# Kernel tuning notes

Measured on AMD Instinct MI355X. Metric: run time of the kernel, lower is better.

## Reference

```python
import jax, jax.numpy as jnp
import numpy as np

B, T, D, H, L, FF, SPLIT = 2, 4096, 256, 4 * 0 + 8, 4, 1024, 2048
HD = D // H
EPS = 1e-5


def _layernorm(x, s, b):
    mu = jnp.mean(x, axis=-1, keepdims=True)
    var = jnp.mean(jnp.square(x - mu), axis=-1, keepdims=True)
    return (x - mu) * jax.lax.rsqrt(var + EPS) * s + b


def setup_inputs() -> dict:
    key = jax.random.key(0)
    ks = jax.random.split(key, 10)
    sc = 0.02
    inp = {
        "rows": jax.random.normal(ks[0], (B, T, D), jnp.float32),
        "train_target_embeddings": jax.random.normal(ks[1], (B, SPLIT, D), jnp.float32),
        "Wq": sc * jax.random.normal(ks[2], (L, D, D), jnp.float32),
        "bq": jnp.zeros((L, D), jnp.float32),
        "Wk": sc * jax.random.normal(ks[3], (L, D, D), jnp.float32),
        "bk": jnp.zeros((L, D), jnp.float32),
        "Wv": sc * jax.random.normal(ks[4], (L, D, D), jnp.float32),
        "bv": jnp.zeros((L, D), jnp.float32),
        "Wo": sc * jax.random.normal(ks[5], (L, D, D), jnp.float32),
        "bo": jnp.zeros((L, D), jnp.float32),
        "W1": sc * jax.random.normal(ks[6], (L, D, FF), jnp.float32),
        "b1": jnp.zeros((L, FF), jnp.float32),
        "W2": sc * jax.random.normal(ks[7], (L, FF, D), jnp.float32),
        "b2": jnp.zeros((L, D), jnp.float32),
        "ln1_s": jnp.ones((L, D), jnp.float32),
        "ln1_b": jnp.zeros((L, D), jnp.float32),
        "ln2_s": jnp.ones((L, D), jnp.float32),
        "ln2_b": jnp.zeros((L, D), jnp.float32),
        "split": SPLIT,
    }
    return inp


def reference(rows, train_target_embeddings, Wq, bq, Wk, bk, Wv, bv, Wo, bo,
              W1, b1, W2, b2, ln1_s, ln1_b, ln2_s, ln2_b, split):
    # residual add of train target embeddings onto the train rows
    x = rows.at[:, :split, :].add(train_target_embeddings)
    t = x.shape[1]
    # allowed mask: every query can see all train columns; test queries also see themselves
    key_is_train = jnp.arange(t) < split                      # [T]
    allowed = key_is_train[None, :] | jnp.eye(t, dtype=bool)  # [T,T]
    neg = jnp.asarray(-1e9, x.dtype)
    scale = 1.0 / np.sqrt(HD)
    n_layers = Wq.shape[0]
    for l in range(n_layers):
        # multi-head attention with structured mask
        q = (x @ Wq[l] + bq[l]).reshape(x.shape[0], t, H, HD)
        k = (x @ Wk[l] + bk[l]).reshape(x.shape[0], t, H, HD)
        v = (x @ Wv[l] + bv[l]).reshape(x.shape[0], t, H, HD)
        logits = jnp.einsum('bqhd,bkhd->bhqk', q, k) * scale
        logits = jnp.where(allowed[None, None], logits, neg)
        attn = jax.nn.softmax(logits, axis=-1)
        o = jnp.einsum('bhqk,bkhd->bqhd', attn, v).reshape(x.shape[0], t, D)
        x = _layernorm(x + (o @ Wo[l] + bo[l]), ln1_s[l], ln1_b[l])
        # feed-forward
        h = jax.nn.gelu(x @ W1[l] + b1[l])
        x = _layernorm(x + (h @ W2[l] + b2[l]), ln2_s[l], ln2_b[l])
    return x
```

## Files before the change

kernel.cpp:

```cpp
#include <hip/hip_runtime.h>
#include <cstdint>
#include <cstddef>

#define TSEQ 4096
#define BATCH 2
#define DIM 256
#define NHEAD 8
#define HDIM 32
#define NLAYER 4
#define FFDIM 1024
#define SPLITN 2048
#define MROWS (BATCH * TSEQ)

#define QSCALE 0.2550784545f

typedef __attribute__((ext_vector_type(4))) float f32x4;
typedef __attribute__((ext_vector_type(8))) short bf16x8;

__device__ __forceinline__ short f2bf(float f) {
  union { float f; uint32_t u; } v; v.f = f;
  uint32_t r = v.u + 0x7fffu + ((v.u >> 16) & 1u);
  return (short)(r >> 16);
}

__device__ __forceinline__ float bf2f(short s) {
  union { uint32_t u; float f; } v; v.u = ((uint32_t)(uint16_t)s) << 16;
  return v.f;
}

__device__ __forceinline__ float fast_exp2(float x) {
#if __has_builtin(__builtin_amdgcn_exp2f)
  return __builtin_amdgcn_exp2f(x);
#else
  float r;
  asm volatile("v_exp_f32 %0, %1\n\ts_nop 1" : "=v"(r) : "v"(x));
  return r;
#endif
}

__device__ __forceinline__ uint32_t pack2bf(float a, float b) {
  union { float f; uint32_t u; } ua, ub; ua.f = a; ub.f = b;
  return ((ua.u + 0x8000u) >> 16) | ((ub.u + 0x8000u) & 0xffff0000u);
}

__device__ __forceinline__ float gelu_f(float x) {
  float u = 0.7978845608f * x * (1.0f + 0.044715f * x * x);
  u = fminf(fmaxf(u, -20.f), 20.f);
  float e = fast_exp2(2.885390082f * u);
  float t = (e - 1.0f) / (e + 1.0f);
  return 0.5f * x * (1.0f + t);
}

#define AS1 __attribute__((address_space(1)))
#define AS3 __attribute__((address_space(3)))
__device__ __forceinline__ void gload16(const void* g, void* l) {
  __builtin_amdgcn_global_load_lds((AS1 void*)g, (AS3 void*)l, 16, 0, 0);
}

__global__ __launch_bounds__(256) void prep_w(
    const float* __restrict__ Wq, const float* __restrict__ Wk,
    const float* __restrict__ Wv, const float* __restrict__ Wo,
    const float* __restrict__ W1, const float* __restrict__ W2,
    short* __restrict__ qkvT, short* __restrict__ woT,
    short* __restrict__ w1T, short* __restrict__ w2T)
{
  const int NQKV = NLAYER * 768 * DIM;
  const int NO   = NLAYER * DIM * DIM;
  const int NF   = NLAYER * FFDIM * DIM;
  const int total = NQKV + NO + 2 * NF;
  for (int idx = blockIdx.x * 256 + threadIdx.x; idx < total; idx += gridDim.x * 256) {
    if (idx < NQKV) {
      const int l = idx / (768 * DIM);
      const int rem = idx - l * 768 * DIM;
      const int n = rem >> 8, k = rem & 255;
      const float* src = (n < 256) ? Wq : ((n < 512) ? Wk : Wv);
      qkvT[idx] = f2bf(src[((size_t)l * DIM + k) * DIM + (n & 255)]);
    } else if (idx < NQKV + NO) {
      const int j = idx - NQKV;
      const int l = j >> 16;
      const int rem = j & 65535;
      const int n = rem >> 8, k = rem & 255;
      woT[j] = f2bf(Wo[((size_t)l * DIM + k) * DIM + n]);
    } else if (idx < NQKV + NO + NF) {
      const int j = idx - NQKV - NO;
      const int l = j >> 18;
      const int rem = j & 262143;
      const int n = rem >> 8, k = rem & 255;
      w1T[j] = f2bf(W1[((size_t)l * DIM + k) * FFDIM + n]);
    } else {
      const int j = idx - NQKV - NO - NF;
      const int l = j >> 18;
      const int rem = j & 262143;
      const int n = rem >> 10, k = rem & 1023;
      w2T[j] = f2bf(W2[((size_t)l * FFDIM + k) * DIM + n]);
    }
  }
}

__global__ __launch_bounds__(256) void prep_x(
    const float* __restrict__ rows, const float* __restrict__ tte,
    float* __restrict__ xf, short* __restrict__ xb)
{
  const size_t idx = (size_t)blockIdx.x * 256 + threadIdx.x;
  float4 v = ((const float4*)rows)[idx];
  const size_t e = idx * 4;
  const int m = (int)(e >> 8);
  const int d = (int)(e & 255);
  const int t = m & (TSEQ - 1);
  const int bb = m >> 12;
  if (t < SPLITN) {
    const float4 a = ((const float4*)tte)[((size_t)bb * SPLITN + t) * (DIM / 4) + (d >> 2)];
    v.x += a.x; v.y += a.y; v.z += a.z; v.w += a.w;
  }
  ((float4*)xf)[idx] = v;
  short4 pk; pk.x = f2bf(v.x); pk.y = f2bf(v.y); pk.z = f2bf(v.z); pk.w = f2bf(v.w);
  ((short4*)xb)[idx] = pk;
}

#define GBM 128
#define GBN 64
#define GBK 64

template<int EPI>
__global__ __launch_bounds__(256, 4) void gemm_bt(
    const short* __restrict__ A, const short* __restrict__ BT,
    const float* __restrict__ bias0, const float* __restrict__ bias1,
    const float* __restrict__ bias2, void* __restrict__ Cout,
    int M, int N, int K)
{
  __shared__ short As[GBM * GBK];
  __shared__ short Bs[GBN * GBK];
  const int tid = threadIdx.x;
  const int lane = tid & 63;
  const int wave = tid >> 6;
  const int wm = wave & 1, wn = wave >> 1;
  const int col = lane & 15, quad = lane >> 4;

  const short* Ab = A + (size_t)blockIdx.x * GBM * K;
  const short* Bb = BT + (size_t)blockIdx.y * GBN * K;

  const f32x4 fz = {0.f, 0.f, 0.f, 0.f};
  f32x4 acc[4][2];
#pragma unroll
  for (int i = 0; i < 4; ++i)
#pragma unroll
    for (int j = 0; j < 2; ++j) acc[i][j] = fz;

  for (int k0 = 0; k0 < K; k0 += GBK) {
#pragma unroll
    for (int p = 0; p < 4; ++p) {
      int i = p * 256 + tid;
      gload16(Ab + (size_t)(i >> 3) * K + k0 + (i & 7) * 8, &As[i * 8]);
    }
#pragma unroll
    for (int p = 0; p < 2; ++p) {
      int i = p * 256 + tid;
      gload16(Bb + (size_t)(i >> 3) * K + k0 + (i & 7) * 8, &Bs[i * 8]);
    }
    __syncthreads();
#pragma unroll
    for (int ks = 0; ks < GBK; ks += 32) {
      bf16x8 af[4], bfr[2];
#pragma unroll
      for (int tm = 0; tm < 4; ++tm)
        af[tm] = *(const bf16x8*)&As[(wm * 64 + tm * 16 + col) * GBK + ks + quad * 8];
#pragma unroll
      for (int tn = 0; tn < 2; ++tn)
        bfr[tn] = *(const bf16x8*)&Bs[(wn * 32 + tn * 16 + col) * GBK + ks + quad * 8];
#pragma unroll
      for (int tm = 0; tm < 4; ++tm)
#pragma unroll
        for (int tn = 0; tn < 2; ++tn)
          acc[tm][tn] = __builtin_amdgcn_mfma_f32_16x16x32_bf16(af[tm], bfr[tn], acc[tm][tn], 0, 0, 0);
    }
    __syncthreads();
  }

#pragma unroll
  for (int tm = 0; tm < 4; ++tm) {
    const int mbase = blockIdx.x * GBM + wm * 64 + tm * 16 + quad * 4;
#pragma unroll
    for (int tn = 0; tn < 2; ++tn) {
      const int n = blockIdx.y * GBN + wn * 32 + tn * 16 + col;
      float bv;
      if (EPI == 1) bv = (n < 256) ? bias0[n] : ((n < 512) ? bias1[n - 256] : bias2[n - 512]);
      else          bv = bias0[n];
#pragma unroll
      for (int r = 0; r < 4; ++r) {
        float v = acc[tm][tn][r] + bv;
        size_t off = (size_t)(mbase + r) * N + n;
        if (EPI == 1) {
          if (n < 256) v *= QSCALE;
          ((short*)Cout)[off] = f2bf(v);
        } else {
          ((short*)Cout)[off] = f2bf(gelu_f(v));
        }
      }
    }
  }
}

template<int MODE>
__global__ __launch_bounds__(256, 3) void gemm_ln(
    const short* __restrict__ A, const float* __restrict__ Opart,
    const float* __restrict__ lpart,
    const short* __restrict__ BT, const float* __restrict__ bias,
    const float* __restrict__ xres,
    const float* __restrict__ gs, const float* __restrict__ gb,
    float* __restrict__ xoutf, short* __restrict__ xoutb, int K)
{
  __shared__ short As[32 * 64];
  __shared__ short Bs[256 * 64];
  __shared__ float ssum[4][32], ssq[4][32];
  const int tid = threadIdx.x;
  const int lane = tid & 63;
  const int wave = tid >> 6;
  const int col = lane & 15, quad = lane >> 4;
  const int m0 = blockIdx.x * 32;

  const f32x4 fz = {0.f, 0.f, 0.f, 0.f};
  f32x4 acc[2][4];
#pragma unroll
  for (int i = 0; i < 2; ++i)
#pragma unroll
    for (int j = 0; j < 4; ++j) acc[i][j] = fz;

  const int arow = tid >> 3;
  const int agr  = tid & 7;
  const int grow = m0 + arow;

  for (int k0 = 0; k0 < K; k0 += 64) {
    if (MODE == 0) {
      const bf16x8 av = *(const bf16x8*)(A + (size_t)grow * K + k0 + agr * 8);
      *(bf16x8*)&As[arow * 64 + ((agr ^ (arow & 7)) * 8)] = av;
    } else {
      const int tt = grow & (TSEQ - 1), bb = grow >> 12;
      const int head = (k0 >> 5) + (agr >= 4 ? 1 : 0);
      const size_t lidx = (size_t)(bb * 8 + head) * TSEQ + tt;
      const float l = lpart[lidx] + lpart[(size_t)16 * TSEQ + lidx];
      const float li = 1.0f / l;
      const size_t obase = (size_t)grow * DIM + k0 + agr * 8;
      const float4 a0 = *(const float4*)(Opart + obase);
      const float4 a1 = *(const float4*)(Opart + obase + 4);
      const float4 c0 = *(const float4*)(Opart + (size_t)MROWS * DIM + obase);
      const float4 c1 = *(const float4*)(Opart + (size_t)MROWS * DIM + obase + 4);
      uint4 w;
      w.x = pack2bf((a0.x + c0.x) * li, (a0.y + c0.y) * li);
      w.y = pack2bf((a0.z + c0.z) * li, (a0.w + c0.w) * li);
      w.z = pack2bf((a1.x + c1.x) * li, (a1.y + c1.y) * li);
      w.w = pack2bf((a1.z + c1.z) * li, (a1.w + c1.w) * li);
      *(uint4*)&As[arow * 64 + ((agr ^ (arow & 7)) * 8)] = w;
    }
#pragma unroll
    for (int p = 0; p < 8; ++p) {
      int i = p * 256 + tid;
      gload16(BT + (size_t)(i >> 3) * K + k0 + (i & 7) * 8, &Bs[i * 8]);
    }
    __syncthreads();
#pragma unroll
    for (int ks = 0; ks < 64; ks += 32) {
      bf16x8 af[2], bfr[4];
#pragma unroll
      for (int tm = 0; tm < 2; ++tm) {
        const int row = tm * 16 + col;
        const int g = (ks >> 3) + quad;
        af[tm] = *(const bf16x8*)&As[row * 64 + ((g ^ (row & 7)) * 8)];
      }
#pragma unroll
      for (int tn = 0; tn < 4; ++tn)
        bfr[tn] = *(const bf16x8*)&Bs[(wave * 64 + tn * 16 + col) * 64 + ks + quad * 8];
#pragma unroll
      for (int tm = 0; tm < 2; ++tm)
#pragma unroll
        for (int tn = 0; tn < 4; ++tn)
          acc[tm][tn] = __builtin_amdgcn_mfma_f32_16x16x32_bf16(af[tm], bfr[tn], acc[tm][tn], 0, 0, 0);
    }
    __syncthreads();
  }

  const float* resb = xres + (size_t)m0 * DIM;
#pragma unroll
  for (int tn = 0; tn < 4; ++tn) {
    const int n = wave * 64 + tn * 16 + col;
    const float bv = bias[n];
#pragma unroll
    for (int tm = 0; tm < 2; ++tm)
#pragma unroll
      for (int r = 0; r < 4; ++r) {
        const int row = tm * 16 + quad * 4 + r;
        acc[tm][tn][r] += bv + resb[(size_t)row * DIM + n];
      }
  }

#pragma unroll
  for (int tm = 0; tm < 2; ++tm)
#pragma unroll
    for (int r = 0; r < 4; ++r) {
      float s = 0.f, q = 0.f;
#pragma unroll
      for (int tn = 0; tn < 4; ++tn) { const float v = acc[tm][tn][r]; s += v; q += v * v; }
      s += __shfl_xor(s, 1); q += __shfl_xor(q, 1);
      s += __shfl_xor(s, 2); q += __shfl_xor(q, 2);
      s += __shfl_xor(s, 4); q += __shfl_xor(q, 4);
      s += __shfl_xor(s, 8); q += __shfl_xor(q, 8);
      if (col == 0) { const int row = tm * 16 + quad * 4 + r; ssum[wave][row] = s; ssq[wave][row] = q; }
    }
  __syncthreads();
  if (tid < 32) {
    const float S = ssum[0][tid] + ssum[1][tid] + ssum[2][tid] + ssum[3][tid];
    const float Q = ssq[0][tid] + ssq[1][tid] + ssq[2][tid] + ssq[3][tid];
    const float mu = S * (1.0f / DIM);
    const float var = Q * (1.0f / DIM) - mu * mu;
    ssum[0][tid] = mu;
    ssq[0][tid] = rsqrtf(var + 1e-5f);
  }
  __syncthreads();

#pragma unroll
  for (int tm = 0; tm < 2; ++tm)
#pragma unroll
    for (int tn = 0; tn < 4; ++tn) {
      const int n = wave * 64 + tn * 16 + col;
      const float g = gs[n], bb = gb[n];
#pragma unroll
      for (int r = 0; r < 4; ++r) {
        const int row = tm * 16 + quad * 4 + r;
        const float out = (acc[tm][tn][r] - ssum[0][row]) * ssq[0][row] * g + bb;
        xoutf[(size_t)(m0 + row) * DIM + n] = out;
        xoutb[(size_t)(m0 + row) * DIM + n] = f2bf(out);
      }
    }
}

#define AKT 64
#define KSPL 1024
#define NKT (KSPL / AKT)

__global__ __launch_bounds__(256, 4) void attn_kernel(
    const short* __restrict__ qkv,
    float* __restrict__ Opart, float* __restrict__ lpart)
{
  __shared__ short Kbuf[2][AKT * HDIM];
  __shared__ short Vbuf[2][HDIM * AKT];
  __shared__ short Pall[4][32][72];
  __shared__ float Pdiag[4][16];

  const int tid = threadIdx.x;
  const int lane = tid & 63;
  const int wave = tid >> 6;
  const int col = lane & 15, quad = lane >> 4;
  const int bh = blockIdx.y;
  const int b = bh >> 3, h = bh & 7;
  const int hz = blockIdx.z;
  const int q0 = blockIdx.x * 128 + wave * 32;

  short (*P)[72] = Pall[wave];

  const short* qbase = qkv + (size_t)b * TSEQ * 768 + h * HDIM;
  const short* kbase = qbase + 256;
  const short* vcol  = qbase + 512;

  const short* ksrc = kbase + (size_t)(hz * KSPL + (tid & 63)) * 768 + (tid >> 6) * 8;
  const int vkey = tid & 63, vhg = tid >> 6;
  const int va = vkey >> 3, vb8 = vkey & 7;
  const short* vsrc = vcol + (size_t)(hz * KSPL + vkey) * 768 + vhg * 8;

  const bf16x8 qf0 = *(const bf16x8*)(qbase + (size_t)(q0 + col) * 768 + quad * 8);
  const bf16x8 qf1 = *(const bf16x8*)(qbase + (size_t)(q0 + 16 + col) * 768 + quad * 8);

  bf16x8 ones;
#pragma unroll
  for (int i = 0; i < 8; ++i) ones[i] = (short)0x3F80;

  const f32x4 fz = {0.f, 0.f, 0.f, 0.f};
  f32x4 o[2][2] = {{fz, fz}, {fz, fz}};
  f32x4 lacc[2] = {fz, fz};

  gload16(ksrc, &Kbuf[0][tid * 8]);
  {
    const bf16x8 v0 = *(const bf16x8*)vsrc;
#pragma unroll
    for (int j = 0; j < 8; ++j)
      Vbuf[0][(vhg * 8 + j) * 64 + ((va ^ j) * 8) + vb8] = v0[j];
  }
  bf16x8 vnext = *(const bf16x8*)(vsrc + (size_t)AKT * 768);

  int cur = 0;
  for (int t = 0; t < NKT; ++t) {
    __syncthreads();
    if (t + 1 < NKT) {
      gload16(ksrc + (size_t)(t + 1) * AKT * 768, &Kbuf[1 - cur][tid * 8]);
#pragma unroll
      for (int j = 0; j < 8; ++j)
        Vbuf[1 - cur][(vhg * 8 + j) * 64 + ((va ^ j) * 8) + vb8] = vnext[j];
      if (t + 2 < NKT) vnext = *(const bf16x8*)(vsrc + (size_t)(t + 2) * AKT * 768);
    }
    const short* kb = Kbuf[cur];
    const short* vb = Vbuf[cur];

#pragma unroll
    for (int st = 0; st < 4; ++st) {
      const bf16x8 kf = *(const bf16x8*)&kb[(quad * 64 + st * 16 + col) * 8];
      const f32x4 s0 = __builtin_amdgcn_mfma_f32_16x16x32_bf16(kf, qf0, fz, 0, 0, 0);
      const f32x4 s1 = __builtin_amdgcn_mfma_f32_16x16x32_bf16(kf, qf1, fz, 0, 0, 0);
      uint2 w0, w1;
      w0.x = pack2bf(fast_exp2(s0[0]), fast_exp2(s0[1]));
      w0.y = pack2bf(fast_exp2(s0[2]), fast_exp2(s0[3]));
      w1.x = pack2bf(fast_exp2(s1[0]), fast_exp2(s1[1]));
      w1.y = pack2bf(fast_exp2(s1[2]), fast_exp2(s1[3]));
      *(uint2*)&P[col][st * 16 + quad * 4] = w0;
      *(uint2*)&P[16 + col][st * 16 + quad * 4] = w1;
    }
    asm volatile("s_waitcnt lgkmcnt(0)" ::: "memory");

#pragma unroll
    for (int kh = 0; kh < 2; ++kh) {
      const bf16x8 pf0 = *(const bf16x8*)&P[col][kh * 32 + quad * 8];
      const bf16x8 pf1 = *(const bf16x8*)&P[16 + col][kh * 32 + quad * 8];
#pragma unroll
      for (int hh = 0; hh < 2; ++hh) {
        const int hd = hh * 16 + col;
        const bf16x8 vf = *(const bf16x8*)&vb[hd * AKT + (((kh * 4 + quad) ^ (hd & 7)) * 8)];
        o[0][hh] = __builtin_amdgcn_mfma_f32_16x16x32_bf16(pf0, vf, o[0][hh], 0, 0, 0);
        o[1][hh] = __builtin_amdgcn_mfma_f32_16x16x32_bf16(pf1, vf, o[1][hh], 0, 0, 0);
      }
      lacc[0] = __builtin_amdgcn_mfma_f32_16x16x32_bf16(pf0, ones, lacc[0], 0, 0, 0);
      lacc[1] = __builtin_amdgcn_mfma_f32_16x16x32_bf16(pf1, ones, lacc[1], 0, 0, 0);
    }
    cur ^= 1;
  }

  if (hz == 1 && blockIdx.x >= SPLITN / 128) {
#pragma unroll
    for (int qsub = 0; qsub < 2; ++qsub) {
      const int qd = q0 + qsub * 16;
      const bf16x8 qf = qsub ? qf1 : qf0;
      const bf16x8 kf = *(const bf16x8*)(kbase + (size_t)(qd + col) * 768 + quad * 8);
      const f32x4 sd = __builtin_amdgcn_mfma_f32_16x16x32_bf16(kf, qf, fz, 0, 0, 0);
      float ps = 0.f;
#pragma unroll
      for (int r = 0; r < 4; ++r)
        if (quad * 4 + r == col) ps = fast_exp2(sd[r]);
      if (quad == (col >> 2)) Pdiag[wave][col] = ps;
      asm volatile("s_waitcnt lgkmcnt(0)" ::: "memory");
      const f32x4 pv = *(const f32x4*)&Pdiag[wave][quad * 4];
#pragma unroll
      for (int r = 0; r < 4; ++r) {
        lacc[qsub][r] += pv[r];
        const size_t vrow = (size_t)(qd + quad * 4 + r) * 768;
#pragma unroll
        for (int hh = 0; hh < 2; ++hh)
          o[qsub][hh][r] += pv[r] * bf2f(vcol[vrow + hh * 16 + col]);
      }
      asm volatile("s_waitcnt lgkmcnt(0)" ::: "memory");
    }
  }

  float* Ob = Opart + (size_t)hz * MROWS * DIM;
  float* lb = lpart + (size_t)hz * 16 * TSEQ + (size_t)bh * TSEQ;
#pragma unroll
  for (int qsub = 0; qsub < 2; ++qsub) {
    const f32x4 la = lacc[qsub];
    const int qq = q0 + qsub * 16 + quad * 4;
    const int rowb = b * TSEQ + qq;
#pragma unroll
    for (int r = 0; r < 4; ++r) {
      if (col == 0) lb[qq + r] = la[r];
#pragma unroll
      for (int hh = 0; hh < 2; ++hh)
        Ob[(size_t)(rowb + r) * DIM + h * HDIM + hh * 16 + col] = o[qsub][hh][r];
    }
  }
}

extern "C" void kernel_launch(void* const* d_in, const int* in_sizes, int n_in,
                              void* d_out, int out_size, void* d_ws, size_t ws_size,
                              hipStream_t stream)
{
  const float* rows = (const float*)d_in[0];
  const float* tte  = (const float*)d_in[1];
  const float* Wq = (const float*)d_in[2];  const float* bq = (const float*)d_in[3];
  const float* Wk = (const float*)d_in[4];  const float* bk = (const float*)d_in[5];
  const float* Wv = (const float*)d_in[6];  const float* bv = (const float*)d_in[7];
  const float* Wo = (const float*)d_in[8];  const float* bo = (const float*)d_in[9];
  const float* W1 = (const float*)d_in[10]; const float* b1 = (const float*)d_in[11];
  const float* W2 = (const float*)d_in[12]; const float* b2 = (const float*)d_in[13];
  const float* ln1s = (const float*)d_in[14]; const float* ln1b = (const float*)d_in[15];
  const float* ln2s = (const float*)d_in[16]; const float* ln2b = (const float*)d_in[17];

  char* p = (char*)d_ws;
  float* xf   = (float*)p;  p += (size_t)MROWS * DIM * 4;
  short* xb   = (short*)p;  p += (size_t)MROWS * DIM * 2;
  short* qkv  = (short*)p;  p += (size_t)MROWS * 768 * 2;
  short* hb   = (short*)p;  p += (size_t)MROWS * FFDIM * 2;
  float* Opart = (float*)p; p += (size_t)2 * MROWS * DIM * 4;
  float* lpart = (float*)p; p += (size_t)2 * 16 * TSEQ * 4;
  short* qkvT = (short*)p;  p += (size_t)NLAYER * 768 * DIM * 2;
  short* woT  = (short*)p;  p += (size_t)NLAYER * DIM * DIM * 2;
  short* w1T  = (short*)p;  p += (size_t)NLAYER * FFDIM * DIM * 2;
  short* w2T  = (short*)p;  p += (size_t)NLAYER * DIM * FFDIM * 2;

  prep_w<<<2048, 256, 0, stream>>>(Wq, Wk, Wv, Wo, W1, W2, qkvT, woT, w1T, w2T);
  prep_x<<<MROWS * DIM / 4 / 256, 256, 0, stream>>>(rows, tte, xf, xb);

  for (int l = 0; l < NLAYER; ++l) {
    gemm_bt<1><<<dim3(MROWS / GBM, 768 / GBN), 256, 0, stream>>>(
        xb, qkvT + (size_t)l * 768 * DIM, bq + l * DIM, bk + l * DIM, bv + l * DIM,
        qkv, MROWS, 768, DIM);
    attn_kernel<<<dim3(TSEQ / 128, BATCH * NHEAD, 2), 256, 0, stream>>>(qkv, Opart, lpart);
    gemm_ln<1><<<MROWS / 32, 256, 0, stream>>>(
        nullptr, Opart, lpart, woT + (size_t)l * DIM * DIM, bo + l * DIM, xf,
        ln1s + l * DIM, ln1b + l * DIM, xf, xb, DIM);
    gemm_bt<3><<<dim3(MROWS / GBM, FFDIM / GBN), 256, 0, stream>>>(
        xb, w1T + (size_t)l * FFDIM * DIM, b1 + l * FFDIM, nullptr, nullptr,
        hb, MROWS, FFDIM, DIM);
    float* xo = (l == NLAYER - 1) ? (float*)d_out : xf;
    gemm_ln<0><<<MROWS / 32, 256, 0, stream>>>(
        hb, nullptr, nullptr, w2T + (size_t)l * DIM * FFDIM,
        b2 + l * DIM, xf, ln2s + l * DIM, ln2b + l * DIM, xo, xb, FFDIM);
  }
}
```

Measured before the change: 518.0 us.

## Double-buffer gemm_ln K loop and XOR-swizzle LDS tiles in both GEMMs

The gemm_ln kernel now uses two LDS buffers. It issues the global loads for the next K tile (B via gload16, A either directly or as Opart/lpart register prefetch) before computing the current tile, so loads overlap MFMA work and one barrier per iteration is removed. Both the plain GEMM and gemm_ln apply an XOR swizzle to the column group when staging into LDS, which reduces bank conflicts on fragment reads. Doubling LDS (about 68KB per block) forces launch_bounds down from 3 to 2 blocks per SM, trading occupancy for overlap.

```diff
diff --git a/kernel.cpp b/kernel.cpp
--- a/kernel.cpp
+++ b/kernel.cpp
@@ -149,24 +149,31 @@
   for (int k0 = 0; k0 < K; k0 += GBK) {
 #pragma unroll
     for (int p = 0; p < 4; ++p) {
-      int i = p * 256 + tid;
-      gload16(Ab + (size_t)(i >> 3) * K + k0 + (i & 7) * 8, &As[i * 8]);
+      const int i = p * 256 + tid;
+      const int r = i >> 3, g = i & 7;
+      gload16(Ab + (size_t)r * K + k0 + ((g ^ (r & 7)) * 8), &As[i * 8]);
     }
 #pragma unroll
     for (int p = 0; p < 2; ++p) {
-      int i = p * 256 + tid;
-      gload16(Bb + (size_t)(i >> 3) * K + k0 + (i & 7) * 8, &Bs[i * 8]);
+      const int i = p * 256 + tid;
+      const int r = i >> 3, g = i & 7;
+      gload16(Bb + (size_t)r * K + k0 + ((g ^ (r & 7)) * 8), &Bs[i * 8]);
     }
     __syncthreads();
 #pragma unroll
     for (int ks = 0; ks < GBK; ks += 32) {
       bf16x8 af[4], bfr[2];
-#pragma unroll
-      for (int tm = 0; tm < 4; ++tm)
-        af[tm] = *(const bf16x8*)&As[(wm * 64 + tm * 16 + col) * GBK + ks + quad * 8];
-#pragma unroll
-      for (int tn = 0; tn < 2; ++tn)
-        bfr[tn] = *(const bf16x8*)&Bs[(wn * 32 + tn * 16 + col) * GBK + ks + quad * 8];
+      const int gq = (ks >> 3) + quad;
+#pragma unroll
+      for (int tm = 0; tm < 4; ++tm) {
+        const int row = wm * 64 + tm * 16 + col;
+        af[tm] = *(const bf16x8*)&As[row * GBK + ((gq ^ (row & 7)) * 8)];
+      }
+#pragma unroll
+      for (int tn = 0; tn < 2; ++tn) {
+        const int row = wn * 32 + tn * 16 + col;
+        bfr[tn] = *(const bf16x8*)&Bs[row * GBK + ((gq ^ (row & 7)) * 8)];
+      }
 #pragma unroll
       for (int tm = 0; tm < 4; ++tm)
 #pragma unroll
@@ -201,7 +208,7 @@
 }
 
 template<int MODE>
-__global__ __launch_bounds__(256, 3) void gemm_ln(
+__global__ __launch_bounds__(256, 2) void gemm_ln(
     const short* __restrict__ A, const float* __restrict__ Opart,
     const float* __restrict__ lpart,
     const short* __restrict__ BT, const float* __restrict__ bias,
@@ -209,8 +216,8 @@
     const float* __restrict__ gs, const float* __restrict__ gb,
     float* __restrict__ xoutf, short* __restrict__ xoutb, int K)
 {
-  __shared__ short As[32 * 64];
-  __shared__ short Bs[256 * 64];
+  __shared__ short As[2][32 * 64];
+  __shared__ short Bs[2][256 * 64];
   __shared__ float ssum[4][32], ssq[4][32];
   const int tid = threadIdx.x;
   const int lane = tid & 63;
@@ -228,55 +235,84 @@
   const int arow = tid >> 3;
   const int agr  = tid & 7;
   const int grow = m0 + arow;
-
-  for (int k0 = 0; k0 < K; k0 += 64) {
-    if (MODE == 0) {
-      const bf16x8 av = *(const bf16x8*)(A + (size_t)grow * K + k0 + agr * 8);
-      *(bf16x8*)&As[arow * 64 + ((agr ^ (arow & 7)) * 8)] = av;
-    } else {
-      const int tt = grow & (TSEQ - 1), bb = grow >> 12;
-      const int head = (k0 >> 5) + (agr >= 4 ? 1 : 0);
-      const size_t lidx = (size_t)(bb * 8 + head) * TSEQ + tt;
-      const float l = lpart[lidx] + lpart[(size_t)16 * TSEQ + lidx];
-      const float li = 1.0f / l;
-      const size_t obase = (size_t)grow * DIM + k0 + agr * 8;
-      const float4 a0 = *(const float4*)(Opart + obase);
-      const float4 a1 = *(const float4*)(Opart + obase + 4);
-      const float4 c0 = *(const float4*)(Opart + (size_t)MROWS * DIM + obase);
-      const float4 c1 = *(const float4*)(Opart + (size_t)MROWS * DIM + obase + 4);
-      uint4 w;
-      w.x = pack2bf((a0.x + c0.x) * li, (a0.y + c0.y) * li);
-      w.y = pack2bf((a0.z + c0.z) * li, (a0.w + c0.w) * li);
-      w.z = pack2bf((a1.x + c1.x) * li, (a1.y + c1.y) * li);
-      w.w = pack2bf((a1.z + c1.z) * li, (a1.w + c1.w) * li);
-      *(uint4*)&As[arow * 64 + ((agr ^ (arow & 7)) * 8)] = w;
-    }
-#pragma unroll
-    for (int p = 0; p < 8; ++p) {
-      int i = p * 256 + tid;
-      gload16(BT + (size_t)(i >> 3) * K + k0 + (i & 7) * 8, &Bs[i * 8]);
-    }
-    __syncthreads();
+  const int asw  = (agr ^ (arow & 7)) * 8;
+
+  float4 sa0, sa1, sc0, sc1; float sli = 0.f;
+
+#define STAGE_B(k0_, buf_) do {                                              \
+    _Pragma("unroll")                                                        \
+    for (int p_ = 0; p_ < 8; ++p_) {                                         \
+      const int i_ = p_ * 256 + tid;                                         \
+      const int r_ = i_ >> 3, g_ = i_ & 7;                                   \
+      gload16(BT + (size_t)r_ * K + (k0_) + ((g_ ^ (r_ & 7)) * 8),           \
+              &Bs[buf_][i_ * 8]);                                            \
+    } } while (0)
+
+#define STAGE_A_ISSUE(k0_, buf_) do {                                        \
+    if (MODE == 0) {                                                         \
+      gload16(A + (size_t)grow * K + (k0_) + asw, &As[buf_][tid * 8]);       \
+    } else {                                                                 \
+      const int tt_ = grow & (TSEQ - 1), bb_ = grow >> 12;                   \
+      const int head_ = ((k0_) >> 5) + (agr >= 4 ? 1 : 0);                   \
+      const size_t lidx_ = (size_t)(bb_ * 8 + head_) * TSEQ + tt_;           \
+      sli = lpart[lidx_] + lpart[(size_t)16 * TSEQ + lidx_];                 \
+      const size_t ob_ = (size_t)grow * DIM + (k0_) + agr * 8;               \
+      sa0 = *(const float4*)(Opart + ob_);                                   \
+      sa1 = *(const float4*)(Opart + ob_ + 4);                               \
+      sc0 = *(const float4*)(Opart + (size_t)MROWS * DIM + ob_);             \
+      sc1 = *(const float4*)(Opart + (size_t)MROWS * DIM + ob_ + 4);         \
+    } } while (0)
+
+#define STAGE_A_WRITE(buf_) do {                                             \
+    if (MODE == 1) {                                                         \
+      const float li_ = 1.0f / sli;                                          \
+      uint4 w_;                                                              \
+      w_.x = pack2bf((sa0.x + sc0.x) * li_, (sa0.y + sc0.y) * li_);          \
+      w_.y = pack2bf((sa0.z + sc0.z) * li_, (sa0.w + sc0.w) * li_);          \
+      w_.z = pack2bf((sa1.x + sc1.x) * li_, (sa1.y + sc1.y) * li_);          \
+      w_.w = pack2bf((sa1.z + sc1.z) * li_, (sa1.w + sc1.w) * li_);          \
+      *(uint4*)&As[buf_][arow * 64 + asw] = w_;                              \
+    } } while (0)
+
+  const int NT = K / 64;
+  STAGE_B(0, 0);
+  STAGE_A_ISSUE(0, 0);
+  STAGE_A_WRITE(0);
+  __syncthreads();
+
+  int cur = 0;
+  for (int t = 0; t < NT; ++t) {
+    if (t + 1 < NT) {
+      STAGE_B((t + 1) * 64, cur ^ 1);
+      STAGE_A_ISSUE((t + 1) * 64, cur ^ 1);
+    }
 #pragma unroll
     for (int ks = 0; ks < 64; ks += 32) {
       bf16x8 af[2], bfr[4];
+      const int gq = (ks >> 3) + quad;
 #pragma unroll
       for (int tm = 0; tm < 2; ++tm) {
         const int row = tm * 16 + col;
-        const int g = (ks >> 3) + quad;
-        af[tm] = *(const bf16x8*)&As[row * 64 + ((g ^ (row & 7)) * 8)];
-      }
-#pragma unroll
-      for (int tn = 0; tn < 4; ++tn)
-        bfr[tn] = *(const bf16x8*)&Bs[(wave * 64 + tn * 16 + col) * 64 + ks + quad * 8];
+        af[tm] = *(const bf16x8*)&As[cur][row * 64 + ((gq ^ (row & 7)) * 8)];
+      }
+#pragma unroll
+      for (int tn = 0; tn < 4; ++tn) {
+        const int row = wave * 64 + tn * 16 + col;
+        bfr[tn] = *(const bf16x8*)&Bs[cur][row * 64 + ((gq ^ (row & 7)) * 8)];
+      }
 #pragma unroll
       for (int tm = 0; tm < 2; ++tm)
 #pragma unroll
         for (int tn = 0; tn < 4; ++tn)
           acc[tm][tn] = __builtin_amdgcn_mfma_f32_16x16x32_bf16(af[tm], bfr[tn], acc[tm][tn], 0, 0, 0);
     }
+    if (t + 1 < NT) STAGE_A_WRITE(cur ^ 1);
     __syncthreads();
-  }
+    cur ^= 1;
+  }
+#undef STAGE_B
+#undef STAGE_A_ISSUE
+#undef STAGE_A_WRITE
 
   const float* resb = xres + (size_t)m0 * DIM;
 #pragma unroll
```

Result: faster. 495.6 us (-4.3%).
